# Performance work log

Measured on AMD Instinct MI355X. Metric: run time of the kernel, lower is better.

The kernel has to match this reference:

```python
import jax, jax.numpy as jnp
import numpy as np

N_ENT = 2000
GAT_EMB = 64
GAT_HID = 3
HIDDEN = 256
BATCH = 8
ALPHA = 0.2  # LeakyReLU negative slope
MASK_FILL = jnp.float32(9e-15)  # original fills masked-out logits with 9e-15 (NOT -inf)


def setup_inputs() -> dict:
    key = jax.random.key(0)
    k1, k2, k3, k4, k5, k6 = jax.random.split(key, 6)
    emb = jax.random.normal(k1, (N_ENT, GAT_EMB), dtype=jnp.float32)
    W = jax.random.normal(k2, (GAT_EMB, GAT_HID), dtype=jnp.float32) * 0.2
    a = jax.random.normal(k3, (2 * GAT_HID, 1), dtype=jnp.float32) * 0.2
    fc1_w = jax.random.normal(k4, (HIDDEN, N_ENT * GAT_HID), dtype=jnp.float32) * 0.02
    fc1_b = jax.random.normal(k5, (HIDDEN,), dtype=jnp.float32) * 0.02
    adj = jax.random.randint(k6, (BATCH, N_ENT, N_ENT), 0, 2, dtype=jnp.int32)
    return {"emb": emb, "W": W, "a": a, "fc1_w": fc1_w, "fc1_b": fc1_b, "adj": adj}


def reference(emb, W, a, fc1_w, fc1_b, adj):
    # h = emb @ W : [N, 3] -- shared across all graphs in the batch
    h = emb @ W
    # Pairwise logits: original concatenates [h_i, h_j] and dots with a;
    # equivalent to (h @ a1)_i + (h @ a2)_j via broadcasting (no O(N^2*2H) tensor).
    s1 = h @ a[:GAT_HID, 0]   # [N]
    s2 = h @ a[GAT_HID:, 0]   # [N]
    e = jax.nn.leaky_relu(s1[:, None] + s2[None, :], negative_slope=ALPHA)  # [N, N]
    # Mask by adjacency (fill 9e-15, matching original), softmax over neighbors (dim=1)
    masked = jnp.where(adj > 0, e[None, :, :], MASK_FILL)  # [B, N, N]
    att = jax.nn.softmax(masked, axis=2)
    # Weighted aggregation + ELU (concat=True head)
    h_prime = jnp.einsum('bij,jd->bid', att, h)  # [B, N, 3]
    x = jax.nn.elu(h_prime).reshape(att.shape[0], -1)  # [B, N*3]
    return x @ fc1_w.T + fc1_b  # [B, hidden]
```

## Files before the change

kernel.cpp:

```cpp
#include <hip/hip_runtime.h>
#include <cstddef>

#define N_ENT   2000
#define GAT_EMB 64
#define HIDDEN  256
#define BATCH   8
#define ALPHA   0.2f

typedef _Float16 half4 __attribute__((ext_vector_type(4)));

#define WS_HX_OFF      8192
#define WS_HY_OFF      12288
#define WS_HZ_OFF      16384
#define WS_S1_OFF      20480
#define WS_TABLE_BYTES 28672
#define WS_X_OFF       28672
#define WS_TIER2_BYTES 124672

__global__ __launch_bounds__(256) void k_init(const float* __restrict__ fc1_b,
                                              float* __restrict__ out) {
    int idx = blockIdx.x * 256 + threadIdx.x;
    out[idx] = fc1_b[idx & (HIDDEN - 1)];
}

__global__ __launch_bounds__(256) void k_prep(const float* __restrict__ emb,
                                              const float* __restrict__ W,
                                              const float* __restrict__ a,
                                              float* __restrict__ ws) {
    __shared__ float sW[GAT_EMB * 3];
    __shared__ float sa[6];
    int t = threadIdx.x;
    if (t < GAT_EMB * 3) sW[t] = W[t];
    if (t < 6)           sa[t] = a[t];
    __syncthreads();
    int i = blockIdx.x * 256 + t;
    if (i >= N_ENT) return;
    const float4* er = (const float4*)(emb + (size_t)i * GAT_EMB);
    float h0 = 0.f, h1 = 0.f, h2 = 0.f;
#pragma unroll
    for (int k4 = 0; k4 < GAT_EMB / 4; ++k4) {
        float4 e4 = er[k4];
        int k = 4 * k4;
        h0 += e4.x * sW[(k + 0) * 3 + 0]; h1 += e4.x * sW[(k + 0) * 3 + 1]; h2 += e4.x * sW[(k + 0) * 3 + 2];
        h0 += e4.y * sW[(k + 1) * 3 + 0]; h1 += e4.y * sW[(k + 1) * 3 + 1]; h2 += e4.y * sW[(k + 1) * 3 + 2];
        h0 += e4.z * sW[(k + 2) * 3 + 0]; h1 += e4.z * sW[(k + 2) * 3 + 1]; h2 += e4.z * sW[(k + 2) * 3 + 2];
        h0 += e4.w * sW[(k + 3) * 3 + 0]; h1 += e4.w * sW[(k + 3) * 3 + 1]; h2 += e4.w * sW[(k + 3) * 3 + 2];
    }
    ws[i] = h0 * sa[3] + h1 * sa[4] + h2 * sa[5];
    ((_Float16*)((char*)ws + WS_HX_OFF))[i] = (_Float16)h0;
    ((_Float16*)((char*)ws + WS_HY_OFF))[i] = (_Float16)h1;
    ((_Float16*)((char*)ws + WS_HZ_OFF))[i] = (_Float16)h2;
    ws[WS_S1_OFF / 4 + i] = h0 * sa[0] + h1 * sa[1] + h2 * sa[2];
}

__global__ __launch_bounds__(256, 4) void k_main(const float* __restrict__ emb,
                                                 const float* __restrict__ W,
                                                 const float* __restrict__ a,
                                                 const float* __restrict__ fc1_w,
                                                 const int*   __restrict__ adj,
                                                 float* __restrict__ wsf,
                                                 int mode,
                                                 float* __restrict__ out) {
    __shared__ __align__(16) unsigned char smem[20480];
    float*    s2s = (float*)smem;
    _Float16* hxs = (_Float16*)(smem + 8192);
    _Float16* hys = (_Float16*)(smem + 12288);
    _Float16* hzs = (_Float16*)(smem + 16384);
    __shared__ float sW[GAT_EMB * 3];
    __shared__ float sa[6];
    __shared__ float s1sh[2];
    __shared__ float xblk[BATCH][8];

    int t  = threadIdx.x;
    int g  = blockIdx.x;
    int i0 = g * 2;

    if (mode != 0) {
        const uint4* src = (const uint4*)wsf;
        uint4* dst = (uint4*)smem;
#pragma unroll
        for (int rep = 0; rep < 5; ++rep) dst[rep * 256 + t] = src[rep * 256 + t];
    } else {
        if (t < GAT_EMB * 3) sW[t] = W[t];
        if (t < 6)           sa[t] = a[t];
        __syncthreads();
        for (int j = t; j < N_ENT; j += 256) {
            const float4* er = (const float4*)(emb + (size_t)j * GAT_EMB);
            float h0 = 0.f, h1 = 0.f, h2 = 0.f;
#pragma unroll
            for (int k4 = 0; k4 < GAT_EMB / 4; ++k4) {
                float4 e4 = er[k4];
                int k = 4 * k4;
                h0 += e4.x * sW[(k + 0) * 3 + 0]; h1 += e4.x * sW[(k + 0) * 3 + 1]; h2 += e4.x * sW[(k + 0) * 3 + 2];
                h0 += e4.y * sW[(k + 1) * 3 + 0]; h1 += e4.y * sW[(k + 1) * 3 + 1]; h2 += e4.y * sW[(k + 1) * 3 + 2];
                h0 += e4.z * sW[(k + 2) * 3 + 0]; h1 += e4.z * sW[(k + 2) * 3 + 1]; h2 += e4.z * sW[(k + 2) * 3 + 2];
                h0 += e4.w * sW[(k + 3) * 3 + 0]; h1 += e4.w * sW[(k + 3) * 3 + 1]; h2 += e4.w * sW[(k + 3) * 3 + 2];
            }
            s2s[j] = h0 * sa[3] + h1 * sa[4] + h2 * sa[5];
            hxs[j] = (_Float16)h0; hys[j] = (_Float16)h1; hzs[j] = (_Float16)h2;
            if (j == i0 || j == i0 + 1)
                s1sh[j - i0] = h0 * sa[0] + h1 * sa[1] + h2 * sa[2];
        }
    }
    if (t < 2048 - N_ENT) {
        int j = N_ENT + t;
        s2s[j] = 0.f; hxs[j] = (_Float16)0; hys[j] = (_Float16)0; hzs[j] = (_Float16)0;
    }
    __syncthreads();

    int lane = t & 63;
    int w    = t >> 6;
    int di   = w >> 1;
    int b0   = (w & 1) * 4;
    int i    = i0 + di;
    float s1v = (mode == 0) ? s1sh[di] : wsf[WS_S1_OFF / 4 + i];

    const int* __restrict__ bp[4];
    float ac0[4], ac1[4], ac2[4], ac3[4];
#pragma unroll
    for (int s = 0; s < 4; ++s) {
        bp[s] = adj + ((size_t)(b0 + s) * N_ENT + i) * N_ENT;
        ac0[s] = 0.f; ac1[s] = 0.f; ac2[s] = 0.f; ac3[s] = 0.f;
    }

#pragma unroll 1
    for (int kk = 0; kk < 4; ++kk) {
        int jA = kk * 512 + (lane << 2);
        int jB = jA + 256;
        bool pB = (jB < N_ENT);
        int jBs = pB ? jB : 0;
        int4 mA[4], mB[4];
#pragma unroll
        for (int s = 0; s < 4; ++s) mA[s] = *(const int4*)(bp[s] + jA);
#pragma unroll
        for (int s = 0; s < 4; ++s) mB[s] = *(const int4*)(bp[s] + jBs);

        float4 s2A = *(const float4*)&s2s[jA];
        float4 s2B = *(const float4*)&s2s[jB];
        half4  hxA = *(const half4*)&hxs[jA], hxB = *(const half4*)&hxs[jB];
        half4  hyA = *(const half4*)&hys[jA], hyB = *(const half4*)&hys[jB];
        half4  hzA = *(const half4*)&hzs[jA], hzB = *(const half4*)&hzs[jB];

        float evA[4], evB[4], hAx[4], hAy[4], hAz[4], hBx[4], hBy[4], hBz[4];
#pragma unroll
        for (int q = 0; q < 4; ++q) {
            float e = s1v + ((const float*)&s2A)[q];
            evA[q] = __expf(fmaxf(e, 0.f) + ALPHA * fminf(e, 0.f));
            float f = s1v + ((const float*)&s2B)[q];
            evB[q] = __expf(fmaxf(f, 0.f) + ALPHA * fminf(f, 0.f));
            hAx[q] = (float)hxA[q]; hAy[q] = (float)hyA[q]; hAz[q] = (float)hzA[q];
            hBx[q] = (float)hxB[q]; hBy[q] = (float)hyB[q]; hBz[q] = (float)hzB[q];
        }
        float zB = pB ? 1.0f : 0.0f;
#pragma unroll
        for (int s = 0; s < 4; ++s) {
            const int* ma = (const int*)&mA[s];
            const int* mb = (const int*)&mB[s];
#pragma unroll
            for (int q = 0; q < 4; ++q) {
                float eA = (ma[q] > 0) ? evA[q] : 1.0f;
                ac0[s] += eA; ac1[s] += eA * hAx[q]; ac2[s] += eA * hAy[q]; ac3[s] += eA * hAz[q];
                float eB = ((mb[q] > 0) ? evB[q] : 1.0f) * zB;
                ac0[s] += eB; ac1[s] += eB * hBx[q]; ac2[s] += eB * hBy[q]; ac3[s] += eB * hBz[q];
            }
        }
    }

#pragma unroll
    for (int off = 32; off > 0; off >>= 1)
#pragma unroll
        for (int s = 0; s < 4; ++s) {
            ac0[s] += __shfl_xor(ac0[s], off, 64);
            ac1[s] += __shfl_xor(ac1[s], off, 64);
            ac2[s] += __shfl_xor(ac2[s], off, 64);
            ac3[s] += __shfl_xor(ac3[s], off, 64);
        }

    if (lane == 0) {
#pragma unroll
        for (int s = 0; s < 4; ++s) {
            float inv = 1.f / ac0[s];
            float p0 = ac1[s] * inv, p1 = ac2[s] * inv, p2 = ac3[s] * inv;
            xblk[b0 + s][3 * di + 0] = (p0 > 0.f) ? p0 : expm1f(p0);
            xblk[b0 + s][3 * di + 1] = (p1 > 0.f) ? p1 : expm1f(p1);
            xblk[b0 + s][3 * di + 2] = (p2 > 0.f) ? p2 : expm1f(p2);
        }
    }
    __syncthreads();

    if (mode == 2) {
        if (t < 48) {
            int b = t & 7, c = t >> 3;
            _Float16* x16 = (_Float16*)((char*)wsf + WS_X_OFF);
            x16[(size_t)(6 * g + c) * 8 + b] = (_Float16)xblk[b][c];
        }
    } else {
        int k = (t + g * 19) & 255;
        const float* wr = fc1_w + (size_t)k * (N_ENT * 3) + 6 * g;
        float2 wA = *(const float2*)wr;
        float2 wB = *(const float2*)(wr + 2);
        float2 wC = *(const float2*)(wr + 4);
#pragma unroll
        for (int b = 0; b < BATCH; ++b) {
            float d = xblk[b][0] * wA.x + xblk[b][1] * wA.y
                    + xblk[b][2] * wB.x + xblk[b][3] * wB.y
                    + xblk[b][4] * wC.x + xblk[b][5] * wC.y;
            atomicAdd(&out[b * HIDDEN + k], d);
        }
    }
}

__global__ __launch_bounds__(256) void k_fc(const _Float16* __restrict__ x16,
                                            const float* __restrict__ fc1_w,
                                            const float* __restrict__ fc1_b,
                                            float* __restrict__ out) {
    int t = threadIdx.x, lane = t & 63, w = t >> 6;
    int k = blockIdx.x * 4 + w;
    const float* __restrict__ wr = fc1_w + (size_t)k * (N_ENT * 3);
    float acc[BATCH];
#pragma unroll
    for (int b = 0; b < BATCH; ++b) acc[b] = 0.f;
#pragma unroll 1
    for (int it = 0; it < 24; ++it) {
        int m0 = it * 256 + (lane << 2);
        if (m0 < N_ENT * 3) {
            float4 wv4 = *(const float4*)(wr + m0);
#pragma unroll
            for (int q = 0; q < 4; ++q) {
                half4 xa = *(const half4*)(x16 + (size_t)(m0 + q) * 8);
                half4 xb = *(const half4*)(x16 + (size_t)(m0 + q) * 8 + 4);
                float wv = ((const float*)&wv4)[q];
                acc[0] += wv * (float)xa[0]; acc[1] += wv * (float)xa[1];
                acc[2] += wv * (float)xa[2]; acc[3] += wv * (float)xa[3];
                acc[4] += wv * (float)xb[0]; acc[5] += wv * (float)xb[1];
                acc[6] += wv * (float)xb[2]; acc[7] += wv * (float)xb[3];
            }
        }
    }
#pragma unroll
    for (int off = 32; off > 0; off >>= 1)
#pragma unroll
        for (int b = 0; b < BATCH; ++b) acc[b] += __shfl_xor(acc[b], off, 64);
    if (lane == 0) {
        float bias = fc1_b[k];
#pragma unroll
        for (int b = 0; b < BATCH; ++b) out[b * HIDDEN + k] = acc[b] + bias;
    }
}

extern "C" void kernel_launch(void* const* d_in, const int* in_sizes, int n_in,
                              void* d_out, int out_size, void* d_ws, size_t ws_size,
                              hipStream_t stream) {
    const float* emb   = (const float*)d_in[0];
    const float* W     = (const float*)d_in[1];
    const float* a     = (const float*)d_in[2];
    const float* fc1_w = (const float*)d_in[3];
    const float* fc1_b = (const float*)d_in[4];
    const int*   adj   = (const int*)d_in[5];
    float* out = (float*)d_out;
    float* ws  = (float*)d_ws;
    (void)in_sizes; (void)n_in; (void)out_size;

    int tier = (ws_size >= (size_t)WS_TIER2_BYTES) ? 2
             : (ws_size >= (size_t)WS_TABLE_BYTES) ? 1 : 0;

    if (tier < 2)  k_init<<<8, 256, 0, stream>>>(fc1_b, out);
    if (tier >= 1) k_prep<<<8, 256, 0, stream>>>(emb, W, a, ws);
    k_main<<<N_ENT / 2, 256, 0, stream>>>(emb, W, a, fc1_w, adj, ws, tier, out);
    if (tier == 2)
        k_fc<<<64, 256, 0, stream>>>((const _Float16*)((char*)d_ws + WS_X_OFF),
                                     fc1_w, fc1_b, out);
}
```

Measured before the change: 226.0 us.

## Remap k_main to one row per block and widen k_fc grid

The main GAT kernel now runs one entity row per block instead of two, across N_ENT blocks. Each wave handles two batches over all 8 column chunks, starting at a staggered phase so that concurrent waves spread their adjacency-stream accesses. Occupancy hint goes from 4 to 5 blocks per CU. The FC kernel now runs one output neuron per block with a shared-memory cross-wave reduction, spreading the fc1_w read over more blocks. The cost is twice as many blocks, each repeating the shared-table load, and fewer independent loads in flight per thread.

Result: faster. 215.2 us (-4.8%).

```diff
diff --git a/kernel.cpp b/kernel.cpp
--- a/kernel.cpp
+++ b/kernel.cpp
@@ -53,7 +53,7 @@
     ws[WS_S1_OFF / 4 + i] = h0 * sa[0] + h1 * sa[1] + h2 * sa[2];
 }
 
-__global__ __launch_bounds__(256, 4) void k_main(const float* __restrict__ emb,
+__global__ __launch_bounds__(256, 5) void k_main(const float* __restrict__ emb,
                                                  const float* __restrict__ W,
                                                  const float* __restrict__ a,
                                                  const float* __restrict__ fc1_w,
@@ -68,12 +68,11 @@
     _Float16* hzs = (_Float16*)(smem + 16384);
     __shared__ float sW[GAT_EMB * 3];
     __shared__ float sa[6];
-    __shared__ float s1sh[2];
-    __shared__ float xblk[BATCH][8];
-
-    int t  = threadIdx.x;
-    int g  = blockIdx.x;
-    int i0 = g * 2;
+    __shared__ float s1sh[1];
+    __shared__ float xblk[BATCH][4];
+
+    int t = threadIdx.x;
+    int g = blockIdx.x;
 
     if (mode != 0) {
         const uint4* src = (const uint4*)wsf;
@@ -98,8 +97,7 @@
             }
             s2s[j] = h0 * sa[3] + h1 * sa[4] + h2 * sa[5];
             hxs[j] = (_Float16)h0; hys[j] = (_Float16)h1; hzs[j] = (_Float16)h2;
-            if (j == i0 || j == i0 + 1)
-                s1sh[j - i0] = h0 * sa[0] + h1 * sa[1] + h2 * sa[2];
+            if (j == g) s1sh[0] = h0 * sa[0] + h1 * sa[1] + h2 * sa[2];
         }
     }
     if (t < 2048 - N_ENT) {
@@ -110,101 +108,80 @@
 
     int lane = t & 63;
     int w    = t >> 6;
-    int di   = w >> 1;
-    int b0   = (w & 1) * 4;
-    int i    = i0 + di;
-    float s1v = (mode == 0) ? s1sh[di] : wsf[WS_S1_OFF / 4 + i];
-
-    const int* __restrict__ bp[4];
-    float ac0[4], ac1[4], ac2[4], ac3[4];
-#pragma unroll
-    for (int s = 0; s < 4; ++s) {
-        bp[s] = adj + ((size_t)(b0 + s) * N_ENT + i) * N_ENT;
-        ac0[s] = 0.f; ac1[s] = 0.f; ac2[s] = 0.f; ac3[s] = 0.f;
-    }
-
-#pragma unroll 1
-    for (int kk = 0; kk < 4; ++kk) {
-        int jA = kk * 512 + (lane << 2);
-        int jB = jA + 256;
-        bool pB = (jB < N_ENT);
-        int jBs = pB ? jB : 0;
-        int4 mA[4], mB[4];
-#pragma unroll
-        for (int s = 0; s < 4; ++s) mA[s] = *(const int4*)(bp[s] + jA);
-#pragma unroll
-        for (int s = 0; s < 4; ++s) mB[s] = *(const int4*)(bp[s] + jBs);
-
-        float4 s2A = *(const float4*)&s2s[jA];
-        float4 s2B = *(const float4*)&s2s[jB];
-        half4  hxA = *(const half4*)&hxs[jA], hxB = *(const half4*)&hxs[jB];
-        half4  hyA = *(const half4*)&hys[jA], hyB = *(const half4*)&hys[jB];
-        half4  hzA = *(const half4*)&hzs[jA], hzB = *(const half4*)&hzs[jB];
-
-        float evA[4], evB[4], hAx[4], hAy[4], hAz[4], hBx[4], hBy[4], hBz[4];
+    float s1v = (mode == 0) ? s1sh[0] : wsf[WS_S1_OFF / 4 + g];
+    const int* __restrict__ baseA = adj + ((size_t)(2 * w + 0) * N_ENT + g) * N_ENT;
+    const int* __restrict__ baseB = adj + ((size_t)(2 * w + 1) * N_ENT + g) * N_ENT;
+    int phase = (g + 3 * w) & 7;
+    int l4 = lane << 2;
+
+    float aA0 = 0.f, aA1 = 0.f, aA2 = 0.f, aA3 = 0.f;
+    float aB0 = 0.f, aB1 = 0.f, aB2 = 0.f, aB3 = 0.f;
+
+#pragma unroll
+    for (int s = 0; s < 8; ++s) {
+        int c  = (s + phase) & 7;
+        int j0 = c * 256 + l4;
+        bool valid = (j0 < N_ENT);
+        int jc = valid ? j0 : 0;
+        int4 mA = *(const int4*)(baseA + jc);
+        int4 mB = *(const int4*)(baseB + jc);
+        float4 s2v = *(const float4*)&s2s[j0];
+        half4  hxv = *(const half4*)&hxs[j0];
+        half4  hyv = *(const half4*)&hys[j0];
+        half4  hzv = *(const half4*)&hzs[j0];
+        float vw = valid ? 1.0f : 0.0f;
+        float ev[4], hx[4], hy[4], hz[4];
 #pragma unroll
         for (int q = 0; q < 4; ++q) {
-            float e = s1v + ((const float*)&s2A)[q];
-            evA[q] = __expf(fmaxf(e, 0.f) + ALPHA * fminf(e, 0.f));
-            float f = s1v + ((const float*)&s2B)[q];
-            evB[q] = __expf(fmaxf(f, 0.f) + ALPHA * fminf(f, 0.f));
-            hAx[q] = (float)hxA[q]; hAy[q] = (float)hyA[q]; hAz[q] = (float)hzA[q];
-            hBx[q] = (float)hxB[q]; hBy[q] = (float)hyB[q]; hBz[q] = (float)hzB[q];
-        }
-        float zB = pB ? 1.0f : 0.0f;
-#pragma unroll
-        for (int s = 0; s < 4; ++s) {
-            const int* ma = (const int*)&mA[s];
-            const int* mb = (const int*)&mB[s];
-#pragma unroll
-            for (int q = 0; q < 4; ++q) {
-                float eA = (ma[q] > 0) ? evA[q] : 1.0f;
-                ac0[s] += eA; ac1[s] += eA * hAx[q]; ac2[s] += eA * hAy[q]; ac3[s] += eA * hAz[q];
-                float eB = ((mb[q] > 0) ? evB[q] : 1.0f) * zB;
-                ac0[s] += eB; ac1[s] += eB * hBx[q]; ac2[s] += eB * hBy[q]; ac3[s] += eB * hBz[q];
-            }
-        }
-    }
-
-#pragma unroll
-    for (int off = 32; off > 0; off >>= 1)
-#pragma unroll
-        for (int s = 0; s < 4; ++s) {
-            ac0[s] += __shfl_xor(ac0[s], off, 64);
-            ac1[s] += __shfl_xor(ac1[s], off, 64);
-            ac2[s] += __shfl_xor(ac2[s], off, 64);
-            ac3[s] += __shfl_xor(ac3[s], off, 64);
-        }
-
+            float e = s1v + ((const float*)&s2v)[q];
+            ev[q] = __expf(fmaxf(e, 0.f) + ALPHA * fminf(e, 0.f)) ;
+            hx[q] = (float)hxv[q]; hy[q] = (float)hyv[q]; hz[q] = (float)hzv[q];
+        }
+        const int* ma = (const int*)&mA;
+        const int* mb = (const int*)&mB;
+#pragma unroll
+        for (int q = 0; q < 4; ++q) {
+            float eA = ((ma[q] > 0) ? ev[q] : 1.0f) * vw;
+            aA0 += eA; aA1 += eA * hx[q]; aA2 += eA * hy[q]; aA3 += eA * hz[q];
+            float eB = ((mb[q] > 0) ? ev[q] : 1.0f) * vw;
+            aB0 += eB; aB1 += eB * hx[q]; aB2 += eB * hy[q]; aB3 += eB * hz[q];
+        }
+    }
+
+#pragma unroll
+    for (int off = 32; off > 0; off >>= 1) {
+        aA0 += __shfl_xor(aA0, off, 64); aA1 += __shfl_xor(aA1, off, 64);
+        aA2 += __shfl_xor(aA2, off, 64); aA3 += __shfl_xor(aA3, off, 64);
+        aB0 += __shfl_xor(aB0, off, 64); aB1 += __shfl_xor(aB1, off, 64);
+        aB2 += __shfl_xor(aB2, off, 64); aB3 += __shfl_xor(aB3, off, 64);
+    }
     if (lane == 0) {
-#pragma unroll
-        for (int s = 0; s < 4; ++s) {
-            float inv = 1.f / ac0[s];
-            float p0 = ac1[s] * inv, p1 = ac2[s] * inv, p2 = ac3[s] * inv;
-            xblk[b0 + s][3 * di + 0] = (p0 > 0.f) ? p0 : expm1f(p0);
-            xblk[b0 + s][3 * di + 1] = (p1 > 0.f) ? p1 : expm1f(p1);
-            xblk[b0 + s][3 * di + 2] = (p2 > 0.f) ? p2 : expm1f(p2);
-        }
+        float inv = 1.f / aA0;
+        float p0 = aA1 * inv, p1 = aA2 * inv, p2 = aA3 * inv;
+        xblk[2 * w + 0][0] = (p0 > 0.f) ? p0 : expm1f(p0);
+        xblk[2 * w + 0][1] = (p1 > 0.f) ? p1 : expm1f(p1);
+        xblk[2 * w + 0][2] = (p2 > 0.f) ? p2 : expm1f(p2);
+        inv = 1.f / aB0;
+        p0 = aB1 * inv; p1 = aB2 * inv; p2 = aB3 * inv;
+        xblk[2 * w + 1][0] = (p0 > 0.f) ? p0 : expm1f(p0);
+        xblk[2 * w + 1][1] = (p1 > 0.f) ? p1 : expm1f(p1);
+        xblk[2 * w + 1][2] = (p2 > 0.f) ? p2 : expm1f(p2);
     }
     __syncthreads();
 
     if (mode == 2) {
-        if (t < 48) {
+        if (t < 24) {
             int b = t & 7, c = t >> 3;
             _Float16* x16 = (_Float16*)((char*)wsf + WS_X_OFF);
-            x16[(size_t)(6 * g + c) * 8 + b] = (_Float16)xblk[b][c];
+            x16[(size_t)(3 * g + c) * 8 + b] = (_Float16)xblk[b][c];
         }
     } else {
         int k = (t + g * 19) & 255;
-        const float* wr = fc1_w + (size_t)k * (N_ENT * 3) + 6 * g;
-        float2 wA = *(const float2*)wr;
-        float2 wB = *(const float2*)(wr + 2);
-        float2 wC = *(const float2*)(wr + 4);
+        const float* wr = fc1_w + (size_t)k * (N_ENT * 3) + 3 * g;
+        float w0 = wr[0], w1 = wr[1], w2 = wr[2];
 #pragma unroll
         for (int b = 0; b < BATCH; ++b) {
-            float d = xblk[b][0] * wA.x + xblk[b][1] * wA.y
-                    + xblk[b][2] * wB.x + xblk[b][3] * wB.y
-                    + xblk[b][4] * wC.x + xblk[b][5] * wC.y;
+            float d = xblk[b][0] * w0 + xblk[b][1] * w1 + xblk[b][2] * w2;
             atomicAdd(&out[b * HIDDEN + k], d);
         }
     }
@@ -214,16 +191,17 @@
                                             const float* __restrict__ fc1_w,
                                             const float* __restrict__ fc1_b,
                                             float* __restrict__ out) {
+    __shared__ float red[4][8];
     int t = threadIdx.x, lane = t & 63, w = t >> 6;
-    int k = blockIdx.x * 4 + w;
+    int k = blockIdx.x;
     const float* __restrict__ wr = fc1_w + (size_t)k * (N_ENT * 3);
     float acc[BATCH];
 #pragma unroll
     for (int b = 0; b < BATCH; ++b) acc[b] = 0.f;
-#pragma unroll 1
-    for (int it = 0; it < 24; ++it) {
-        int m0 = it * 256 + (lane << 2);
-        if (m0 < N_ENT * 3) {
+#pragma unroll
+    for (int it = 0; it < 6; ++it) {
+        int m0 = 4 * t + 1024 * it;
+        if (m0 + 3 < N_ENT * 3) {
             float4 wv4 = *(const float4*)(wr + m0);
 #pragma unroll
             for (int q = 0; q < 4; ++q) {
@@ -241,10 +219,13 @@
     for (int off = 32; off > 0; off >>= 1)
 #pragma unroll
         for (int b = 0; b < BATCH; ++b) acc[b] += __shfl_xor(acc[b], off, 64);
-    if (lane == 0) {
-        float bias = fc1_b[k];
-#pragma unroll
-        for (int b = 0; b < BATCH; ++b) out[b * HIDDEN + k] = acc[b] + bias;
+    if (lane == 0)
+#pragma unroll
+        for (int b = 0; b < BATCH; ++b) red[w][b] = acc[b];
+    __syncthreads();
+    if (t < 8) {
+        float s = red[0][t] + red[1][t] + red[2][t] + red[3][t] + fc1_b[k];
+        out[t * HIDDEN + k] = s;
     }
 }
 
@@ -266,8 +247,8 @@
 
     if (tier < 2)  k_init<<<8, 256, 0, stream>>>(fc1_b, out);
     if (tier >= 1) k_prep<<<8, 256, 0, stream>>>(emb, W, a, ws);
-    k_main<<<N_ENT / 2, 256, 0, stream>>>(emb, W, a, fc1_w, adj, ws, tier, out);
+    k_main<<<N_ENT, 256, 0, stream>>>(emb, W, a, fc1_w, adj, ws, tier, out);
     if (tier == 2)
-        k_fc<<<64, 256, 0, stream>>>((const _Float16*)((char*)d_ws + WS_X_OFF),
-                                     fc1_w, fc1_b, out);
-}
+        k_fc<<<HIDDEN, 256, 0, stream>>>((const _Float16*)((char*)d_ws + WS_X_OFF),
+                                         fc1_w, fc1_b, out);
+}
```
